# Kernel tuning notes

Measured on AMD Instinct MI355X. Metric: run time of the kernel, lower is better.

The kernel has to match this reference:

```python
import jax, jax.numpy as jnp
import numpy as np

D = 1024      # query_dim
H = 16        # heads
DH = 64       # dim_head
I = H * DH    # inner_dim = 1024
DC = 768      # context_dim
FF = 4 * D    # ff inner dim = 4096
EPS = 1e-5
SCALE = DH ** -0.5


def setup_inputs() -> dict:
    key = jax.random.key(0)
    ks = jax.random.split(key, 20)
    s = 0.02
    inp = {
        'x': jax.random.normal(ks[0], (2, 2048, D), jnp.float32),
        'context': jax.random.normal(ks[1], (2, 77, DC), jnp.float32),
        'ln1_g': jnp.ones((D,), jnp.float32), 'ln1_b': jnp.zeros((D,), jnp.float32),
        'ln2_g': jnp.ones((D,), jnp.float32), 'ln2_b': jnp.zeros((D,), jnp.float32),
        'ln3_g': jnp.ones((D,), jnp.float32), 'ln3_b': jnp.zeros((D,), jnp.float32),
        'Wq1': jax.random.normal(ks[2], (D, I), jnp.float32) * s,
        'Wk1': jax.random.normal(ks[3], (D, I), jnp.float32) * s,
        'Wv1': jax.random.normal(ks[4], (D, I), jnp.float32) * s,
        'Wo1': jax.random.normal(ks[5], (I, D), jnp.float32) * s,
        'bo1': jnp.zeros((D,), jnp.float32),
        'Wq2': jax.random.normal(ks[6], (D, I), jnp.float32) * s,
        'Wk2': jax.random.normal(ks[7], (DC, I), jnp.float32) * s,
        'Wv2': jax.random.normal(ks[8], (DC, I), jnp.float32) * s,
        'Wo2': jax.random.normal(ks[9], (I, D), jnp.float32) * s,
        'bo2': jnp.zeros((D,), jnp.float32),
        'Wff1': jax.random.normal(ks[10], (D, 2 * FF), jnp.float32) * s,
        'bff1': jnp.zeros((2 * FF,), jnp.float32),
        'Wff2': jax.random.normal(ks[11], (FF, D), jnp.float32) * s,
        'bff2': jnp.zeros((D,), jnp.float32),
    }
    return inp


def layer_norm(x, g, b):
    m = jnp.mean(x, axis=-1, keepdims=True)
    v = jnp.mean(jnp.square(x - m), axis=-1, keepdims=True)
    return (x - m) * jax.lax.rsqrt(v + EPS) * g + b


def cross_attention(x, ctx, Wq, Wk, Wv, Wo, bo):
    # x: [B,N,D], ctx: [B,M,Dc]
    B, N, _ = x.shape
    M = ctx.shape[1]
    q = (x @ Wq).reshape(B, N, H, DH).transpose(0, 2, 1, 3)    # [B,H,N,DH]
    k = (ctx @ Wk).reshape(B, M, H, DH).transpose(0, 2, 1, 3)  # [B,H,M,DH]
    v = (ctx @ Wv).reshape(B, M, H, DH).transpose(0, 2, 1, 3)
    sim = jnp.einsum('bhid,bhjd->bhij', q, k) * SCALE           # [B,H,N,M]
    attn = jax.nn.softmax(sim, axis=-1)
    out = jnp.einsum('bhij,bhjd->bhid', attn, v)                # [B,H,N,DH]
    out = out.transpose(0, 2, 1, 3).reshape(B, N, I)
    return out @ Wo + bo


def reference(x, context, ln1_g, ln1_b, ln2_g, ln2_b, ln3_g, ln3_b,
              Wq1, Wk1, Wv1, Wo1, bo1, Wq2, Wk2, Wv2, Wo2, bo2,
              Wff1, bff1, Wff2, bff2):
    # self-attention
    x = cross_attention(layer_norm(x, ln1_g, ln1_b), layer_norm(x, ln1_g, ln1_b),
                        Wq1, Wk1, Wv1, Wo1, bo1) + x
    # cross-attention
    x = cross_attention(layer_norm(x, ln2_g, ln2_b), context,
                        Wq2, Wk2, Wv2, Wo2, bo2) + x
    # GEGLU feed-forward
    hg = layer_norm(x, ln3_g, ln3_b) @ Wff1 + bff1
    h, gate = hg[..., :FF], hg[..., FF:]
    ff = (h * jax.nn.gelu(gate, approximate=False)) @ Wff2 + bff2
    return ff + x
```

## Files before the change

kernel.cpp:

```cpp
#include <hip/hip_runtime.h>
#include <hip/hip_bf16.h>
#include <math.h>

typedef short short8 __attribute__((ext_vector_type(8)));
typedef float floatx4 __attribute__((ext_vector_type(4)));
typedef unsigned short u16;

#define D_MODEL 1024
#define NH 16
#define DH 64
#define FF_DIM 4096

__device__ __forceinline__ u16 f2b(float f) {
  union { float f; unsigned u; } v; v.f = f;
  unsigned r = (v.u + 0x7fffu + ((v.u >> 16) & 1u)) >> 16;
  return (u16)r;
}
__device__ __forceinline__ u16 f2b_fast(float f) {
  union { float f; unsigned u; } v; v.f = f;
  return (u16)((v.u + 0x8000u) >> 16);
}
__device__ __forceinline__ float b2f(u16 h) {
  union { unsigned u; float f; } v; v.u = ((unsigned)h) << 16;
  return v.f;
}

__device__ __forceinline__ void gl_lds16(const u16* g, u16* l) {
  __builtin_amdgcn_global_load_lds(
      (const __attribute__((address_space(1))) unsigned int*)g,
      (__attribute__((address_space(3))) unsigned int*)l, 16, 0, 0);
}

__launch_bounds__(256)
__global__ void transpose_to_bf16(const float* __restrict__ in, u16* __restrict__ out,
                                  int K, int N, float scale) {
  __shared__ float tile[32][33];
  const int n0 = blockIdx.x * 32;
  const int k0 = blockIdx.y * 32;
  const int tx = threadIdx.x & 31;
  const int ty = threadIdx.x >> 5;
#pragma unroll
  for (int i = 0; i < 4; i++) {
    int k = k0 + ty + i * 8;
    tile[ty + i * 8][tx] = in[(size_t)k * N + (n0 + tx)] * scale;
  }
  __syncthreads();
#pragma unroll
  for (int i = 0; i < 4; i++) {
    int n = n0 + ty + i * 8;
    out[(size_t)n * K + (k0 + tx)] = f2b(tile[tx][ty + i * 8]);
  }
}

__launch_bounds__(256)
__global__ void convert_bf16(const float* __restrict__ in, u16* __restrict__ out, int n) {
  int i = blockIdx.x * 256 + threadIdx.x;
  if (i < n) out[i] = f2b(in[i]);
}

__launch_bounds__(256)
__global__ void ln_to_bf16(const float* __restrict__ x, const float* __restrict__ g,
                           const float* __restrict__ b, u16* __restrict__ out) {
  const int row = blockIdx.x;
  const int tid = threadIdx.x;
  const float4 v = ((const float4*)(x + (size_t)row * D_MODEL))[tid];
  float s = v.x + v.y + v.z + v.w;
  float ss = v.x * v.x + v.y * v.y + v.z * v.z + v.w * v.w;
#pragma unroll
  for (int o = 32; o; o >>= 1) { s += __shfl_xor(s, o); ss += __shfl_xor(ss, o); }
  __shared__ float red[8];
  const int wave = tid >> 6, lane = tid & 63;
  if (lane == 0) { red[wave] = s; red[4 + wave] = ss; }
  __syncthreads();
  const float st = red[0] + red[1] + red[2] + red[3];
  const float sst = red[4] + red[5] + red[6] + red[7];
  const float mean = st * (1.0f / D_MODEL);
  const float var = sst * (1.0f / D_MODEL) - mean * mean;
  const float rs = rsqrtf(var + 1e-5f);
  const float4 gv = ((const float4*)g)[tid];
  const float4 bv = ((const float4*)b)[tid];
  ushort4 o4;
  o4.x = f2b((v.x - mean) * rs * gv.x + bv.x);
  o4.y = f2b((v.y - mean) * rs * gv.y + bv.y);
  o4.z = f2b((v.z - mean) * rs * gv.z + bv.z);
  o4.w = f2b((v.w - mean) * rs * gv.w + bv.w);
  ((ushort4*)(out + (size_t)row * D_MODEL))[tid] = o4;
}

template <int EPI>
__launch_bounds__(256)
__global__ void gemm128(const u16* __restrict__ A, const u16* __restrict__ BT,
                        const float* __restrict__ bias, const float* __restrict__ resid,
                        float* __restrict__ Cf, u16* __restrict__ Cb, u16* __restrict__ VT,
                        int K, int lda, int ldb, int ldc) {
  __shared__ __attribute__((aligned(16))) u16 Al[128 * 32];
  __shared__ __attribute__((aligned(16))) u16 Bl[128 * 32];
  const int tid = threadIdx.x, wave = tid >> 6, lane = tid & 63;
  const int lm = lane & 15, lq = lane >> 4;
  const int wr = (wave >> 1) * 64, wc = (wave & 1) * 64;
  const int m0 = blockIdx.y * 128, n0 = blockIdx.x * 128;

  floatx4 acc[4][4] = {};

  for (int k0 = 0; k0 < K; k0 += 32) {
#pragma unroll
    for (int it = 0; it < 2; it++) {
      const int c = wave * 128 + it * 64 + lane;
      const int r = c >> 2, s = c & 3;
      gl_lds16(A + (size_t)(m0 + r) * lda + k0 + s * 8, &Al[c * 8]);
      gl_lds16(BT + (size_t)(n0 + r) * ldb + k0 + s * 8, &Bl[c * 8]);
    }
    __syncthreads();
    short8 af[4], bf[4];
#pragma unroll
    for (int r = 0; r < 4; r++) af[r] = *(const short8*)(&Al[(wr + r * 16 + lm) * 32 + lq * 8]);
#pragma unroll
    for (int c = 0; c < 4; c++) bf[c] = *(const short8*)(&Bl[(wc + c * 16 + lm) * 32 + lq * 8]);
#pragma unroll
    for (int r = 0; r < 4; r++)
#pragma unroll
      for (int c = 0; c < 4; c++)
        acc[r][c] = __builtin_amdgcn_mfma_f32_16x16x32_bf16(af[r], bf[c], acc[r][c], 0, 0, 0);
    __syncthreads();
  }

#pragma unroll
  for (int r = 0; r < 4; r++)
#pragma unroll
    for (int c = 0; c < 4; c++) {
      const int col = n0 + wc + c * 16 + lm;
      const int row0 = m0 + wr + r * 16 + lq * 4;
      if (EPI == 0) {
#pragma unroll
        for (int i = 0; i < 4; i++)
          Cb[(size_t)(row0 + i) * ldc + col] = f2b(acc[r][c][i]);
      } else if (EPI == 1) {
#pragma unroll
        for (int i = 0; i < 4; i++)
          Cf[(size_t)(row0 + i) * ldc + col] =
              acc[r][c][i] + bias[col] + resid[(size_t)(row0 + i) * ldc + col];
      } else {
        if (col < 2048) {
#pragma unroll
          for (int i = 0; i < 4; i++)
            Cb[(size_t)(row0 + i) * ldc + col] = f2b(acc[r][c][i]);
        } else {
          const int d = col - 2048;
          ushort4 pk;
          pk.x = f2b(acc[r][c][0]); pk.y = f2b(acc[r][c][1]);
          pk.z = f2b(acc[r][c][2]); pk.w = f2b(acc[r][c][3]);
          *(ushort4*)(&VT[((size_t)((row0 >> 11) * 1024 + d)) * 2048 + (row0 & 2047)]) = pk;
        }
      }
    }
}

__launch_bounds__(256)
__global__ void gemm_geglu(const u16* __restrict__ A, const u16* __restrict__ BT,
                           const float* __restrict__ bias, u16* __restrict__ Cb,
                           int K, int lda, int ldb) {
  __shared__ __attribute__((aligned(16))) u16 Al[128 * 32];
  __shared__ __attribute__((aligned(16))) u16 Bl[64 * 32];
  __shared__ __attribute__((aligned(16))) u16 Bg[64 * 32];
  const int tid = threadIdx.x, wave = tid >> 6, lane = tid & 63;
  const int lm = lane & 15, lq = lane >> 4;
  const int wr = (wave >> 1) * 64, wc = (wave & 1) * 32;
  const int m0 = blockIdx.y * 128, n0 = blockIdx.x * 64;

  floatx4 acc[4][2] = {};
  floatx4 accg[4][2] = {};

  for (int k0 = 0; k0 < K; k0 += 32) {
#pragma unroll
    for (int it = 0; it < 2; it++) {
      const int c = wave * 128 + it * 64 + lane;
      const int r = c >> 2, s = c & 3;
      gl_lds16(A + (size_t)(m0 + r) * lda + k0 + s * 8, &Al[c * 8]);
    }
    {
      const int c = wave * 64 + lane;
      const int r = c >> 2, s = c & 3;
      gl_lds16(BT + (size_t)(n0 + r) * ldb + k0 + s * 8, &Bl[c * 8]);
      gl_lds16(BT + (size_t)(n0 + r + FF_DIM) * ldb + k0 + s * 8, &Bg[c * 8]);
    }
    __syncthreads();
    short8 af[4], bf[2], bg[2];
#pragma unroll
    for (int r = 0; r < 4; r++) af[r] = *(const short8*)(&Al[(wr + r * 16 + lm) * 32 + lq * 8]);
#pragma unroll
    for (int c = 0; c < 2; c++) {
      bf[c] = *(const short8*)(&Bl[(wc + c * 16 + lm) * 32 + lq * 8]);
      bg[c] = *(const short8*)(&Bg[(wc + c * 16 + lm) * 32 + lq * 8]);
    }
#pragma unroll
    for (int r = 0; r < 4; r++)
#pragma unroll
      for (int c = 0; c < 2; c++) {
        acc[r][c] = __builtin_amdgcn_mfma_f32_16x16x32_bf16(af[r], bf[c], acc[r][c], 0, 0, 0);
        accg[r][c] = __builtin_amdgcn_mfma_f32_16x16x32_bf16(af[r], bg[c], accg[r][c], 0, 0, 0);
      }
    __syncthreads();
  }

#pragma unroll
  for (int r = 0; r < 4; r++)
#pragma unroll
    for (int c = 0; c < 2; c++) {
      const int col = n0 + wc + c * 16 + lm;
#pragma unroll
      for (int i = 0; i < 4; i++) {
        const int row = m0 + wr + r * 16 + lq * 4 + i;
        const float h = acc[r][c][i] + bias[col];
        const float gt = accg[r][c][i] + bias[col + FF_DIM];
        const float gl = 0.5f * gt * (1.0f + erff(gt * 0.70710678118f));
        Cb[(size_t)row * FF_DIM + col] = f2b(h * gl);
      }
    }
}

#define BM 64
#define BN 64
#define LSTR 40

template <int TRANS>
__launch_bounds__(256)
__global__ void gemm_bt64(const u16* __restrict__ A, const u16* __restrict__ BT,
                          u16* __restrict__ Cb,
                          int M, int N, int K, int lda, int ldb, int ldc, int rowsPerB) {
  __shared__ __attribute__((aligned(16))) u16 Al[BM * LSTR];
  __shared__ __attribute__((aligned(16))) u16 Bl[BN * LSTR];
  const int tid = threadIdx.x, wave = tid >> 6, lane = tid & 63;
  const int wm = (wave >> 1) * 32, wn = (wave & 1) * 32;
  const int lm = lane & 15, lq = lane >> 4;
  const int m0 = blockIdx.y * BM, n0 = blockIdx.x * BN;

  floatx4 acc[2][2] = {};
  const int srow = tid >> 2;
  const int scol = (tid & 3) * 8;
  const bool a_ok = (m0 + srow) < M;

  for (int k0 = 0; k0 < K; k0 += 32) {
    int4 av = make_int4(0, 0, 0, 0);
    if (a_ok) av = *(const int4*)(A + (size_t)(m0 + srow) * lda + k0 + scol);
    *(int4*)(&Al[srow * LSTR + scol]) = av;
    int4 bv = *(const int4*)(BT + (size_t)(n0 + srow) * ldb + k0 + scol);
    *(int4*)(&Bl[srow * LSTR + scol]) = bv;
    __syncthreads();
    short8 af[2], bfr[2];
#pragma unroll
    for (int r = 0; r < 2; r++) af[r] = *(const short8*)(&Al[(wm + r * 16 + lm) * LSTR + lq * 8]);
#pragma unroll
    for (int c = 0; c < 2; c++) bfr[c] = *(const short8*)(&Bl[(wn + c * 16 + lm) * LSTR + lq * 8]);
#pragma unroll
    for (int r = 0; r < 2; r++)
#pragma unroll
      for (int c = 0; c < 2; c++)
        acc[r][c] = __builtin_amdgcn_mfma_f32_16x16x32_bf16(af[r], bfr[c], acc[r][c], 0, 0, 0);
    __syncthreads();
  }

#pragma unroll
  for (int r = 0; r < 2; r++)
#pragma unroll
    for (int c = 0; c < 2; c++) {
      const int col = n0 + wn + c * 16 + lm;
#pragma unroll
      for (int i = 0; i < 4; i++) {
        const int row = m0 + wm + r * 16 + lq * 4 + i;
        if (row < M) {
          if (TRANS == 0) {
            Cb[(size_t)row * ldc + col] = f2b(acc[r][c][i]);
          } else {
            const int bb = row / rowsPerB;
            const int n = row - bb * rowsPerB;
            Cb[((size_t)(bb * 1024 + col)) * 128 + n] = f2b(acc[r][c][i]);
          }
        }
      }
    }
}

__launch_bounds__(256)
__global__ void attn_mfma(const u16* __restrict__ Qg, const u16* __restrict__ Kg,
                          const u16* __restrict__ VTg, u16* __restrict__ Ob,
                          int N, int Mk, int kRowsPerBatch, int ldq, int ldk, int vtld) {
  const int ntiles = N / 64;
  const int bh = blockIdx.x / ntiles;
  const int qt = blockIdx.x % ntiles;
  const int b = bh / NH, h = bh % NH;
  const int tid = threadIdx.x, wave = tid >> 6, lane = tid & 63;
  const int lm = lane & 15, lq = lane >> 4;

  __shared__ __attribute__((aligned(16))) u16 Qs[64 * 64];
  __shared__ __attribute__((aligned(16))) u16 Ks[64 * 64];
  __shared__ __attribute__((aligned(16))) u16 Vt[64 * 64];
  __shared__ __attribute__((aligned(16))) u16 Ps[4][16 * 72];

  const u16* Qh = Qg + (size_t)b * N * ldq + h * DH;
  const u16* Kh = Kg + (size_t)b * kRowsPerBatch * ldk + h * DH;
  const u16* Vh = VTg + (size_t)(b * 1024 + h * DH) * vtld;

  {
    const u16* qsrc = Qh + (size_t)qt * 64 * ldq;
#pragma unroll
    for (int it = 0; it < 2; it++) {
      const int c = wave * 128 + it * 64 + lane;
      const int r = c >> 3, p = c & 7, lc = p ^ (r & 7);
      gl_lds16(qsrc + (size_t)r * ldq + lc * 8, &Qs[c * 8]);
    }
  }
  __syncthreads();
  short8 qf[2];
  qf[0] = *(const short8*)(&Qs[(wave * 16 + lm) * 64 + ((lq) ^ (lm & 7)) * 8]);
  qf[1] = *(const short8*)(&Qs[(wave * 16 + lm) * 64 + ((4 + lq) ^ (lm & 7)) * 8]);

  float lpart[4] = {0.f, 0.f, 0.f, 0.f};
  floatx4 o[4] = {};

  for (int kt = 0; kt < Mk; kt += 64) {
    __syncthreads();
    {
      const u16* ksrc = Kh + (size_t)kt * ldk;
      const u16* vsrc = Vh + kt;
#pragma unroll
      for (int it = 0; it < 2; it++) {
        const int c = wave * 128 + it * 64 + lane;
        const int r = c >> 3, p = c & 7, lc = p ^ (r & 7);
        gl_lds16(ksrc + (size_t)r * ldk + lc * 8, &Ks[c * 8]);
        gl_lds16(vsrc + (size_t)r * vtld + lc * 8, &Vt[c * 8]);
      }
    }
    __syncthreads();

    floatx4 s[4];
#pragma unroll
    for (int ct = 0; ct < 4; ct++) {
      short8 kf0 = *(const short8*)(&Ks[(ct * 16 + lm) * 64 + ((lq) ^ (lm & 7)) * 8]);
      short8 kf1 = *(const short8*)(&Ks[(ct * 16 + lm) * 64 + ((4 + lq) ^ (lm & 7)) * 8]);
      floatx4 z = {};
      z = __builtin_amdgcn_mfma_f32_16x16x32_bf16(qf[0], kf0, z, 0, 0, 0);
      z = __builtin_amdgcn_mfma_f32_16x16x32_bf16(qf[1], kf1, z, 0, 0, 0);
      s[ct] = z;
    }

    if (kt + 64 <= Mk) {
#pragma unroll
      for (int reg = 0; reg < 4; reg++) {
        float p0 = __expf(s[0][reg] - 16.0f);
        float p1 = __expf(s[1][reg] - 16.0f);
        float p2 = __expf(s[2][reg] - 16.0f);
        float p3 = __expf(s[3][reg] - 16.0f);
        lpart[reg] += (p0 + p1) + (p2 + p3);
        const int prow = (lq * 4 + reg) * 72;
        Ps[wave][prow + lm] = f2b_fast(p0);
        Ps[wave][prow + 16 + lm] = f2b_fast(p1);
        Ps[wave][prow + 32 + lm] = f2b_fast(p2);
        Ps[wave][prow + 48 + lm] = f2b_fast(p3);
      }
    } else {
#pragma unroll
      for (int reg = 0; reg < 4; reg++) {
        const int prow = (lq * 4 + reg) * 72;
        float psum = 0.f;
#pragma unroll
        for (int ct = 0; ct < 4; ct++) {
          const bool valid = (kt + ct * 16 + lm) < Mk;
          float p = valid ? __expf(s[ct][reg] - 16.0f) : 0.f;
          psum += p;
          Ps[wave][prow + ct * 16 + lm] = f2b_fast(p);
        }
        lpart[reg] += psum;
      }
    }

    const short8 pf0 = *(const short8*)(&Ps[wave][lm * 72 + lq * 8]);
    const short8 pf1 = *(const short8*)(&Ps[wave][lm * 72 + 32 + lq * 8]);
#pragma unroll
    for (int ct = 0; ct < 4; ct++) {
      short8 vf0 = *(const short8*)(&Vt[(ct * 16 + lm) * 64 + ((lq) ^ (lm & 7)) * 8]);
      short8 vf1 = *(const short8*)(&Vt[(ct * 16 + lm) * 64 + ((4 + lq) ^ (lm & 7)) * 8]);
      o[ct] = __builtin_amdgcn_mfma_f32_16x16x32_bf16(pf0, vf0, o[ct], 0, 0, 0);
      o[ct] = __builtin_amdgcn_mfma_f32_16x16x32_bf16(pf1, vf1, o[ct], 0, 0, 0);
    }
  }

  float inv[4];
#pragma unroll
  for (int reg = 0; reg < 4; reg++) {
    float l = lpart[reg];
    l += __shfl_xor(l, 1); l += __shfl_xor(l, 2);
    l += __shfl_xor(l, 4); l += __shfl_xor(l, 8);
    inv[reg] = 1.0f / l;
  }
#pragma unroll
  for (int ct = 0; ct < 4; ct++)
#pragma unroll
    for (int reg = 0; reg < 4; reg++) {
      const int grow = qt * 64 + wave * 16 + lq * 4 + reg;
      Ob[((size_t)(b * N + grow)) * D_MODEL + h * DH + ct * 16 + lm] =
          f2b(o[ct][reg] * inv[reg]);
    }
}

extern "C" void kernel_launch(void* const* d_in, const int* in_sizes, int n_in,
                              void* d_out, int out_size, void* d_ws, size_t ws_size,
                              hipStream_t stream) {
  const float* x    = (const float*)d_in[0];
  const float* ctx  = (const float*)d_in[1];
  const float* ln1g = (const float*)d_in[2];
  const float* ln1b = (const float*)d_in[3];
  const float* ln2g = (const float*)d_in[4];
  const float* ln2b = (const float*)d_in[5];
  const float* ln3g = (const float*)d_in[6];
  const float* ln3b = (const float*)d_in[7];
  const float* Wq1  = (const float*)d_in[8];
  const float* Wk1  = (const float*)d_in[9];
  const float* Wv1  = (const float*)d_in[10];
  const float* Wo1  = (const float*)d_in[11];
  const float* bo1  = (const float*)d_in[12];
  const float* Wq2  = (const float*)d_in[13];
  const float* Wk2  = (const float*)d_in[14];
  const float* Wv2  = (const float*)d_in[15];
  const float* Wo2  = (const float*)d_in[16];
  const float* bo2  = (const float*)d_in[17];
  const float* Wff1 = (const float*)d_in[18];
  const float* bff1 = (const float*)d_in[19];
  const float* Wff2 = (const float*)d_in[20];
  const float* bff2 = (const float*)d_in[21];
  float* out = (float*)d_out;

  char* ws = (char*)d_ws;
  size_t off = 0;
  auto alloc = [&](size_t bytes) -> char* {
    char* p = ws + off;
    off += (bytes + 255) & ~(size_t)255;
    return p;
  };
  u16* wqkv1T = (u16*)alloc((size_t)3072 * 1024 * 2);
  u16* wo1T   = (u16*)alloc((size_t)1024 * 1024 * 2);
  u16* wq2T   = (u16*)alloc((size_t)1024 * 1024 * 2);
  u16* wk2T   = (u16*)alloc((size_t)1024 * 768 * 2);
  u16* wv2T   = (u16*)alloc((size_t)1024 * 768 * 2);
  u16* wo2T   = (u16*)alloc((size_t)1024 * 1024 * 2);
  u16* wff1T  = (u16*)alloc((size_t)8192 * 1024 * 2);
  u16* wff2T  = (u16*)alloc((size_t)1024 * 4096 * 2);
  u16* xln    = (u16*)alloc((size_t)4096 * 1024 * 2);
  u16* ctxb   = (u16*)alloc((size_t)154 * 768 * 2);
  u16* QKVb   = (u16*)alloc((size_t)4096 * 3072 * 2);
  u16* VTb    = (u16*)alloc((size_t)2048 * 2048 * 2);
  u16* K2b    = (u16*)alloc((size_t)256 * 1024 * 2);
  u16* VT2b   = (u16*)alloc((size_t)2048 * 128 * 2);
  u16* Ob     = (u16*)alloc((size_t)4096 * 1024 * 2);
  float* x1   = (float*)alloc((size_t)4096 * 1024 * 4);
  float* x2   = (float*)alloc((size_t)4096 * 1024 * 4);
  u16* ffin   = (u16*)alloc((size_t)4096 * 4096 * 2);
  u16* Q2b    = ffin;

  dim3 blk(256);

  transpose_to_bf16<<<dim3(32, 32), blk, 0, stream>>>(Wq1, wqkv1T, 1024, 1024, 1.0f);
  transpose_to_bf16<<<dim3(32, 32), blk, 0, stream>>>(Wk1, wqkv1T + (size_t)1024 * 1024, 1024, 1024, 0.125f);
  transpose_to_bf16<<<dim3(32, 32), blk, 0, stream>>>(Wv1, wqkv1T + (size_t)2048 * 1024, 1024, 1024, 1.0f);
  transpose_to_bf16<<<dim3(32, 32), blk, 0, stream>>>(Wo1, wo1T, 1024, 1024, 1.0f);
  transpose_to_bf16<<<dim3(32, 32), blk, 0, stream>>>(Wq2, wq2T, 1024, 1024, 1.0f);
  transpose_to_bf16<<<dim3(32, 24), blk, 0, stream>>>(Wk2, wk2T, 768, 1024, 0.125f);
  transpose_to_bf16<<<dim3(32, 24), blk, 0, stream>>>(Wv2, wv2T, 768, 1024, 1.0f);
  transpose_to_bf16<<<dim3(32, 32), blk, 0, stream>>>(Wo2, wo2T, 1024, 1024, 1.0f);
  transpose_to_bf16<<<dim3(256, 32), blk, 0, stream>>>(Wff1, wff1T, 1024, 8192, 1.0f);
  transpose_to_bf16<<<dim3(32, 128), blk, 0, stream>>>(Wff2, wff2T, 4096, 1024, 1.0f);
  convert_bf16<<<(154 * 768 + 255) / 256, blk, 0, stream>>>(ctx, ctxb, 154 * 768);

  ln_to_bf16<<<4096, blk, 0, stream>>>(x, ln1g, ln1b, xln);
  gemm128<2><<<dim3(24, 32), blk, 0, stream>>>(xln, wqkv1T, nullptr, nullptr, nullptr, QKVb,
                                               VTb, 1024, 1024, 1024, 3072);
  attn_mfma<<<2 * NH * (2048 / 64), blk, 0, stream>>>(QKVb, QKVb + 1024, VTb, Ob,
                                                      2048, 2048, 2048, 3072, 3072, 2048);
  gemm128<1><<<dim3(8, 32), blk, 0, stream>>>(Ob, wo1T, bo1, x, x1, nullptr, nullptr,
                                              1024, 1024, 1024, 1024);

  ln_to_bf16<<<4096, blk, 0, stream>>>(x1, ln2g, ln2b, xln);
  gemm128<0><<<dim3(8, 32), blk, 0, stream>>>(xln, wq2T, nullptr, nullptr, nullptr, Q2b,
                                              nullptr, 1024, 1024, 1024, 1024);
  gemm_bt64<0><<<dim3(16, 3), blk, 0, stream>>>(ctxb, wk2T, K2b, 154, 1024, 768, 768, 768, 1024, 77);
  gemm_bt64<1><<<dim3(16, 3), blk, 0, stream>>>(ctxb, wv2T, VT2b, 154, 1024, 768, 768, 768, 1024, 77);
  attn_mfma<<<2 * NH * (2048 / 64), blk, 0, stream>>>(Q2b, K2b, VT2b, Ob,
                                                      2048, 77, 77, 1024, 1024, 128);
  gemm128<1><<<dim3(8, 32), blk, 0, stream>>>(Ob, wo2T, bo2, x1, x2, nullptr, nullptr,
                                              1024, 1024, 1024, 1024);

  ln_to_bf16<<<4096, blk, 0, stream>>>(x2, ln3g, ln3b, xln);
  gemm_geglu<<<dim3(64, 32), blk, 0, stream>>>(xln, wff1T, bff1, ffin, 1024, 1024, 1024);
  gemm128<1><<<dim3(8, 32), blk, 0, stream>>>(ffin, wff2T, bff2, x2, out, nullptr, nullptr,
                                              4096, 4096, 4096, 1024);
}
```

Before: 606.8 us.

## Pre-swizzle weights into MFMA fragment layout and load B directly to registers

All weight transposes and the context conversion are merged into one prep kernel. It writes weights in a per-lane MFMA fragment-tiled layout, so the GEMMs load B operands straight from global memory into registers with one step of double buffering, with no LDS staging for B. The GEGLU epilogue swaps exact erf GELU for the tanh approximation written as a sigmoid via __expf, which changes numerics slightly. It also reallocates buffers so Q2 gets its own buffer and ffin reuses QKVb.

After: 639.1 us. 1.05x slower.

```diff
diff --git a/kernel.cpp b/kernel.cpp
--- a/kernel.cpp
+++ b/kernel.cpp
@@ -11,6 +11,14 @@
 #define DH 64
 #define FF_DIM 4096
 
+#define O_QKV 0
+#define O_O1  3145728
+#define O_Q2  4194304
+#define O_O2  5242880
+#define O_FF1 6291456
+#define O_FF2 14680064
+#define WS_TOTAL 18874368
+
 __device__ __forceinline__ u16 f2b(float f) {
   union { float f; unsigned u; } v; v.f = f;
   unsigned r = (v.u + 0x7fffu + ((v.u >> 16) & 1u)) >> 16;
@@ -20,10 +28,6 @@
   union { float f; unsigned u; } v; v.f = f;
   return (u16)((v.u + 0x8000u) >> 16);
 }
-__device__ __forceinline__ float b2f(u16 h) {
-  union { unsigned u; float f; } v; v.u = ((unsigned)h) << 16;
-  return v.f;
-}
 
 __device__ __forceinline__ void gl_lds16(const u16* g, u16* l) {
   __builtin_amdgcn_global_load_lds(
@@ -32,30 +36,71 @@
 }
 
 __launch_bounds__(256)
-__global__ void transpose_to_bf16(const float* __restrict__ in, u16* __restrict__ out,
-                                  int K, int N, float scale) {
-  __shared__ float tile[32][33];
-  const int n0 = blockIdx.x * 32;
-  const int k0 = blockIdx.y * 32;
-  const int tx = threadIdx.x & 31;
-  const int ty = threadIdx.x >> 5;
-#pragma unroll
-  for (int i = 0; i < 4; i++) {
-    int k = k0 + ty + i * 8;
-    tile[ty + i * 8][tx] = in[(size_t)k * N + (n0 + tx)] * scale;
-  }
-  __syncthreads();
-#pragma unroll
-  for (int i = 0; i < 4; i++) {
-    int n = n0 + ty + i * 8;
-    out[(size_t)n * K + (k0 + tx)] = f2b(tile[tx][ty + i * 8]);
-  }
-}
-
-__launch_bounds__(256)
-__global__ void convert_bf16(const float* __restrict__ in, u16* __restrict__ out, int n) {
-  int i = blockIdx.x * 256 + threadIdx.x;
-  if (i < n) out[i] = f2b(in[i]);
+__global__ void prep_all(const float* __restrict__ Wq1, const float* __restrict__ Wk1,
+                         const float* __restrict__ Wv1, const float* __restrict__ Wo1,
+                         const float* __restrict__ Wq2, const float* __restrict__ Wo2,
+                         const float* __restrict__ Wff1, const float* __restrict__ Wff2,
+                         const float* __restrict__ Wk2, const float* __restrict__ Wv2,
+                         const float* __restrict__ ctx,
+                         u16* __restrict__ ws, u16* __restrict__ wk2T,
+                         u16* __restrict__ wv2T, u16* __restrict__ ctxb) {
+  const int p = blockIdx.x * 4 + (threadIdx.x >> 6);
+  const int lane = threadIdx.x & 63;
+  const int lm = lane & 15, lq = lane >> 4;
+  union { short8 v; u16 u[8]; } ob;
+
+  if (p < 6144) {
+    const int pl = p, kt = pl & 31;
+    const int n = (pl >> 5) * 16 + lm, k0 = kt * 32 + lq * 8;
+    const float* src; int nl; float s;
+    if (n < 1024) { src = Wq1; nl = n; s = 1.f; }
+    else if (n < 2048) { src = Wk1; nl = n - 1024; s = 0.125f; }
+    else { src = Wv1; nl = n - 2048; s = 1.f; }
+#pragma unroll
+    for (int j = 0; j < 8; j++) ob.u[j] = f2b(src[(size_t)(k0 + j) * 1024 + nl] * s);
+    *(short8*)(ws + O_QKV + (size_t)pl * 512 + lane * 8) = ob.v;
+  } else if (p < 12288) {
+    const int pl = (p - 6144) & 2047;
+    const int which = (p - 6144) >> 11;
+    const float* src = (which == 0) ? Wo1 : (which == 1) ? Wq2 : Wo2;
+    const size_t dof = (which == 0) ? O_O1 : (which == 1) ? O_Q2 : O_O2;
+    const int kt = pl & 31;
+    const int n = (pl >> 5) * 16 + lm, k0 = kt * 32 + lq * 8;
+#pragma unroll
+    for (int j = 0; j < 8; j++) ob.u[j] = f2b(src[(size_t)(k0 + j) * 1024 + n]);
+    *(short8*)(ws + dof + (size_t)pl * 512 + lane * 8) = ob.v;
+  } else if (p < 28672) {
+    const int pl = p - 12288;
+    const int kt = pl & 31;
+    const int n = (pl >> 5) * 16 + lm, k0 = kt * 32 + lq * 8;
+#pragma unroll
+    for (int j = 0; j < 8; j++) ob.u[j] = f2b(Wff1[(size_t)(k0 + j) * 8192 + n]);
+    *(short8*)(ws + O_FF1 + (size_t)pl * 512 + lane * 8) = ob.v;
+  } else if (p < 36864) {
+    const int pl = p - 28672;
+    const int kt = pl & 127;
+    const int n = (pl >> 7) * 16 + lm, k0 = kt * 32 + lq * 8;
+#pragma unroll
+    for (int j = 0; j < 8; j++) ob.u[j] = f2b(Wff2[(size_t)(k0 + j) * 1024 + n]);
+    *(short8*)(ws + O_FF2 + (size_t)pl * 512 + lane * 8) = ob.v;
+  } else if (p < 39936) {
+    const int pl = (p - 36864) % 1536;
+    const bool isK = (p - 36864) < 1536;
+    const float* src = isK ? Wk2 : Wv2;
+    const float s = isK ? 0.125f : 1.f;
+    u16* dst = isK ? wk2T : wv2T;
+    const int nt = pl / 24, kt = pl - nt * 24;
+    const int n = nt * 16 + lm, k0 = kt * 32 + lq * 8;
+#pragma unroll
+    for (int j = 0; j < 8; j++) ob.u[j] = f2b(src[(size_t)(k0 + j) * 1024 + n] * s);
+    *(short8*)(dst + (size_t)n * 768 + k0) = ob.v;
+  } else if (p < 40167) {
+    const int pl = p - 39936;
+    const size_t idx = (size_t)pl * 512 + lane * 8;
+#pragma unroll
+    for (int j = 0; j < 8; j++) ob.u[j] = f2b(ctx[idx + j]);
+    *(short8*)(ctxb + idx) = ob.v;
+  }
 }
 
 __launch_bounds__(256)
@@ -89,38 +134,65 @@
 
 template <int EPI>
 __launch_bounds__(256)
-__global__ void gemm128(const u16* __restrict__ A, const u16* __restrict__ BT,
+__global__ void gemm128(const u16* __restrict__ A, const u16* __restrict__ WS,
                         const float* __restrict__ bias, const float* __restrict__ resid,
                         float* __restrict__ Cf, u16* __restrict__ Cb, u16* __restrict__ VT,
-                        int K, int lda, int ldb, int ldc) {
+                        int KT, int lda, int ldc) {
   __shared__ __attribute__((aligned(16))) u16 Al[128 * 32];
-  __shared__ __attribute__((aligned(16))) u16 Bl[128 * 32];
   const int tid = threadIdx.x, wave = tid >> 6, lane = tid & 63;
   const int lm = lane & 15, lq = lane >> 4;
   const int wr = (wave >> 1) * 64, wc = (wave & 1) * 64;
   const int m0 = blockIdx.y * 128, n0 = blockIdx.x * 128;
 
+  const u16* wsb = WS + ((size_t)((n0 >> 4) + (wave & 1) * 4) * KT) * 512 + lane * 8;
   floatx4 acc[4][4] = {};
-
-  for (int k0 = 0; k0 < K; k0 += 32) {
+  short8 b0[4], b1[4];
+
+#pragma unroll
+  for (int c = 0; c < 4; c++) b0[c] = *(const short8*)(wsb + (size_t)(c * KT) * 512);
+
+  for (int kt = 0; kt < KT; kt += 2) {
 #pragma unroll
     for (int it = 0; it < 2; it++) {
       const int c = wave * 128 + it * 64 + lane;
       const int r = c >> 2, s = c & 3;
-      gl_lds16(A + (size_t)(m0 + r) * lda + k0 + s * 8, &Al[c * 8]);
-      gl_lds16(BT + (size_t)(n0 + r) * ldb + k0 + s * 8, &Bl[c * 8]);
-    }
-    __syncthreads();
-    short8 af[4], bf[4];
-#pragma unroll
-    for (int r = 0; r < 4; r++) af[r] = *(const short8*)(&Al[(wr + r * 16 + lm) * 32 + lq * 8]);
-#pragma unroll
-    for (int c = 0; c < 4; c++) bf[c] = *(const short8*)(&Bl[(wc + c * 16 + lm) * 32 + lq * 8]);
-#pragma unroll
-    for (int r = 0; r < 4; r++)
-#pragma unroll
-      for (int c = 0; c < 4; c++)
-        acc[r][c] = __builtin_amdgcn_mfma_f32_16x16x32_bf16(af[r], bf[c], acc[r][c], 0, 0, 0);
+      gl_lds16(A + (size_t)(m0 + r) * lda + kt * 32 + s * 8, &Al[c * 8]);
+    }
+#pragma unroll
+    for (int c = 0; c < 4; c++) b1[c] = *(const short8*)(wsb + (size_t)(c * KT + kt + 1) * 512);
+    __syncthreads();
+    {
+      short8 af[4];
+#pragma unroll
+      for (int r = 0; r < 4; r++) af[r] = *(const short8*)(&Al[(wr + r * 16 + lm) * 32 + lq * 8]);
+#pragma unroll
+      for (int r = 0; r < 4; r++)
+#pragma unroll
+        for (int c = 0; c < 4; c++)
+          acc[r][c] = __builtin_amdgcn_mfma_f32_16x16x32_bf16(af[r], b0[c], acc[r][c], 0, 0, 0);
+    }
+    __syncthreads();
+#pragma unroll
+    for (int it = 0; it < 2; it++) {
+      const int c = wave * 128 + it * 64 + lane;
+      const int r = c >> 2, s = c & 3;
+      gl_lds16(A + (size_t)(m0 + r) * lda + (kt + 1) * 32 + s * 8, &Al[c * 8]);
+    }
+    if (kt + 2 < KT) {
+#pragma unroll
+      for (int c = 0; c < 4; c++) b0[c] = *(const short8*)(wsb + (size_t)(c * KT + kt + 2) * 512);
+    }
+    __syncthreads();
+    {
+      short8 af[4];
+#pragma unroll
+      for (int r = 0; r < 4; r++) af[r] = *(const short8*)(&Al[(wr + r * 16 + lm) * 32 + lq * 8]);
+#pragma unroll
+      for (int r = 0; r < 4; r++)
+#pragma unroll
+        for (int c = 0; c < 4; c++)
+          acc[r][c] = __builtin_amdgcn_mfma_f32_16x16x32_bf16(af[r], b1[c], acc[r][c], 0, 0, 0);
+    }
     __syncthreads();
   }
 
@@ -156,49 +228,79 @@
 }
 
 __launch_bounds__(256)
-__global__ void gemm_geglu(const u16* __restrict__ A, const u16* __restrict__ BT,
+__global__ void gemm_geglu(const u16* __restrict__ A, const u16* __restrict__ WS,
                            const float* __restrict__ bias, u16* __restrict__ Cb,
-                           int K, int lda, int ldb) {
+                           int KT, int lda) {
   __shared__ __attribute__((aligned(16))) u16 Al[128 * 32];
-  __shared__ __attribute__((aligned(16))) u16 Bl[64 * 32];
-  __shared__ __attribute__((aligned(16))) u16 Bg[64 * 32];
   const int tid = threadIdx.x, wave = tid >> 6, lane = tid & 63;
   const int lm = lane & 15, lq = lane >> 4;
   const int wr = (wave >> 1) * 64, wc = (wave & 1) * 32;
   const int m0 = blockIdx.y * 128, n0 = blockIdx.x * 64;
 
+  const u16* wsh = WS + ((size_t)((n0 >> 4) + (wave & 1) * 2) * KT) * 512 + lane * 8;
+  const u16* wsg = wsh + (size_t)256 * KT * 512;
   floatx4 acc[4][2] = {};
   floatx4 accg[4][2] = {};
-
-  for (int k0 = 0; k0 < K; k0 += 32) {
+  short8 bh0[2], bg0[2], bh1[2], bg1[2];
+
+#pragma unroll
+  for (int c = 0; c < 2; c++) {
+    bh0[c] = *(const short8*)(wsh + (size_t)(c * KT) * 512);
+    bg0[c] = *(const short8*)(wsg + (size_t)(c * KT) * 512);
+  }
+
+  for (int kt = 0; kt < KT; kt += 2) {
 #pragma unroll
     for (int it = 0; it < 2; it++) {
       const int c = wave * 128 + it * 64 + lane;
       const int r = c >> 2, s = c & 3;
-      gl_lds16(A + (size_t)(m0 + r) * lda + k0 + s * 8, &Al[c * 8]);
-    }
+      gl_lds16(A + (size_t)(m0 + r) * lda + kt * 32 + s * 8, &Al[c * 8]);
+    }
+#pragma unroll
+    for (int c = 0; c < 2; c++) {
+      bh1[c] = *(const short8*)(wsh + (size_t)(c * KT + kt + 1) * 512);
+      bg1[c] = *(const short8*)(wsg + (size_t)(c * KT + kt + 1) * 512);
+    }
+    __syncthreads();
     {
-      const int c = wave * 64 + lane;
+      short8 af[4];
+#pragma unroll
+      for (int r = 0; r < 4; r++) af[r] = *(const short8*)(&Al[(wr + r * 16 + lm) * 32 + lq * 8]);
+#pragma unroll
+      for (int r = 0; r < 4; r++)
+#pragma unroll
+        for (int c = 0; c < 2; c++) {
+          acc[r][c] = __builtin_amdgcn_mfma_f32_16x16x32_bf16(af[r], bh0[c], acc[r][c], 0, 0, 0);
+          accg[r][c] = __builtin_amdgcn_mfma_f32_16x16x32_bf16(af[r], bg0[c], accg[r][c], 0, 0, 0);
+        }
+    }
+    __syncthreads();
+#pragma unroll
+    for (int it = 0; it < 2; it++) {
+      const int c = wave * 128 + it * 64 + lane;
       const int r = c >> 2, s = c & 3;
-      gl_lds16(BT + (size_t)(n0 + r) * ldb + k0 + s * 8, &Bl[c * 8]);
-      gl_lds16(BT + (size_t)(n0 + r + FF_DIM) * ldb + k0 + s * 8, &Bg[c * 8]);
-    }
-    __syncthreads();
-    short8 af[4], bf[2], bg[2];
-#pragma unroll
-    for (int r = 0; r < 4; r++) af[r] = *(const short8*)(&Al[(wr + r * 16 + lm) * 32 + lq * 8]);
-#pragma unroll
-    for (int c = 0; c < 2; c++) {
-      bf[c] = *(const short8*)(&Bl[(wc + c * 16 + lm) * 32 + lq * 8]);
-      bg[c] = *(const short8*)(&Bg[(wc + c * 16 + lm) * 32 + lq * 8]);
-    }
-#pragma unroll
-    for (int r = 0; r < 4; r++)
+      gl_lds16(A + (size_t)(m0 + r) * lda + (kt + 1) * 32 + s * 8, &Al[c * 8]);
+    }
+    if (kt + 2 < KT) {
 #pragma unroll
       for (int c = 0; c < 2; c++) {
-        acc[r][c] = __builtin_amdgcn_mfma_f32_16x16x32_bf16(af[r], bf[c], acc[r][c], 0, 0, 0);
-        accg[r][c] = __builtin_amdgcn_mfma_f32_16x16x32_bf16(af[r], bg[c], accg[r][c], 0, 0, 0);
-      }
+        bh0[c] = *(const short8*)(wsh + (size_t)(c * KT + kt + 2) * 512);
+        bg0[c] = *(const short8*)(wsg + (size_t)(c * KT + kt + 2) * 512);
+      }
+    }
+    __syncthreads();
+    {
+      short8 af[4];
+#pragma unroll
+      for (int r = 0; r < 4; r++) af[r] = *(const short8*)(&Al[(wr + r * 16 + lm) * 32 + lq * 8]);
+#pragma unroll
+      for (int r = 0; r < 4; r++)
+#pragma unroll
+        for (int c = 0; c < 2; c++) {
+          acc[r][c] = __builtin_amdgcn_mfma_f32_16x16x32_bf16(af[r], bh1[c], acc[r][c], 0, 0, 0);
+          accg[r][c] = __builtin_amdgcn_mfma_f32_16x16x32_bf16(af[r], bg1[c], accg[r][c], 0, 0, 0);
+        }
+    }
     __syncthreads();
   }
 
@@ -212,7 +314,8 @@
         const int row = m0 + wr + r * 16 + lq * 4 + i;
         const float h = acc[r][c][i] + bias[col];
         const float gt = accg[r][c][i] + bias[col + FF_DIM];
-        const float gl = 0.5f * gt * (1.0f + erff(gt * 0.70710678118f));
+        const float z = 1.5957691216f * (gt + 0.044715f * gt * gt * gt);
+        const float gl = gt / (1.0f + __expf(-z));
         Cb[(size_t)row * FF_DIM + col] = f2b(h * gl);
       }
     }
@@ -305,7 +408,7 @@
 #pragma unroll
     for (int it = 0; it < 2; it++) {
       const int c = wave * 128 + it * 64 + lane;
-      const int r = c >> 3, p = c & 7, lc = p ^ (r & 7);
+      const int r = c >> 3, pp = c & 7, lc = pp ^ (r & 7);
       gl_lds16(qsrc + (size_t)r * ldq + lc * 8, &Qs[c * 8]);
     }
   }
@@ -325,7 +428,7 @@
 #pragma unroll
       for (int it = 0; it < 2; it++) {
         const int c = wave * 128 + it * 64 + lane;
-        const int r = c >> 3, p = c & 7, lc = p ^ (r & 7);
+        const int r = c >> 3, pp = c & 7, lc = pp ^ (r & 7);
         gl_lds16(ksrc + (size_t)r * ldk + lc * 8, &Ks[c * 8]);
         gl_lds16(vsrc + (size_t)r * vtld + lc * 8, &Vt[c * 8]);
       }
@@ -365,9 +468,9 @@
 #pragma unroll
         for (int ct = 0; ct < 4; ct++) {
           const bool valid = (kt + ct * 16 + lm) < Mk;
-          float p = valid ? __expf(s[ct][reg] - 16.0f) : 0.f;
-          psum += p;
-          Ps[wave][prow + ct * 16 + lm] = f2b_fast(p);
+          float pv = valid ? __expf(s[ct][reg] - 16.0f) : 0.f;
+          psum += pv;
+          Ps[wave][prow + ct * 16 + lm] = f2b_fast(pv);
         }
         lpart[reg] += psum;
       }
@@ -436,60 +539,46 @@
     off += (bytes + 255) & ~(size_t)255;
     return p;
   };
-  u16* wqkv1T = (u16*)alloc((size_t)3072 * 1024 * 2);
-  u16* wo1T   = (u16*)alloc((size_t)1024 * 1024 * 2);
-  u16* wq2T   = (u16*)alloc((size_t)1024 * 1024 * 2);
-  u16* wk2T   = (u16*)alloc((size_t)1024 * 768 * 2);
-  u16* wv2T   = (u16*)alloc((size_t)1024 * 768 * 2);
-  u16* wo2T   = (u16*)alloc((size_t)1024 * 1024 * 2);
-  u16* wff1T  = (u16*)alloc((size_t)8192 * 1024 * 2);
-  u16* wff2T  = (u16*)alloc((size_t)1024 * 4096 * 2);
-  u16* xln    = (u16*)alloc((size_t)4096 * 1024 * 2);
-  u16* ctxb   = (u16*)alloc((size_t)154 * 768 * 2);
-  u16* QKVb   = (u16*)alloc((size_t)4096 * 3072 * 2);
-  u16* VTb    = (u16*)alloc((size_t)2048 * 2048 * 2);
-  u16* K2b    = (u16*)alloc((size_t)256 * 1024 * 2);
-  u16* VT2b   = (u16*)alloc((size_t)2048 * 128 * 2);
-  u16* Ob     = (u16*)alloc((size_t)4096 * 1024 * 2);
-  float* x1   = (float*)alloc((size_t)4096 * 1024 * 4);
-  float* x2   = (float*)alloc((size_t)4096 * 1024 * 4);
-  u16* ffin   = (u16*)alloc((size_t)4096 * 4096 * 2);
-  u16* Q2b    = ffin;
+  u16* wsAll = (u16*)alloc((size_t)WS_TOTAL * 2);
+  u16* wk2T  = (u16*)alloc((size_t)1024 * 768 * 2);
+  u16* wv2T  = (u16*)alloc((size_t)1024 * 768 * 2);
+  u16* ctxb  = (u16*)alloc((size_t)154 * 768 * 2);
+  u16* xln   = (u16*)alloc((size_t)4096 * 1024 * 2);
+  u16* QKVb  = (u16*)alloc((size_t)4096 * 3072 * 2);
+  u16* VTb   = (u16*)alloc((size_t)2048 * 2048 * 2);
+  u16* K2b   = (u16*)alloc((size_t)256 * 1024 * 2);
+  u16* VT2b  = (u16*)alloc((size_t)2048 * 128 * 2);
+  u16* Ob    = (u16*)alloc((size_t)4096 * 1024 * 2);
+  u16* Q2b   = (u16*)alloc((size_t)4096 * 1024 * 2);
+  float* x1  = (float*)alloc((size_t)4096 * 1024 * 4);
+  float* x2  = (float*)alloc((size_t)4096 * 1024 * 4);
+  u16* ffin  = QKVb;
 
   dim3 blk(256);
 
-  transpose_to_bf16<<<dim3(32, 32), blk, 0, stream>>>(Wq1, wqkv1T, 1024, 1024, 1.0f);
-  transpose_to_bf16<<<dim3(32, 32), blk, 0, stream>>>(Wk1, wqkv1T + (size_t)1024 * 1024, 1024, 1024, 0.125f);
-  transpose_to_bf16<<<dim3(32, 32), blk, 0, stream>>>(Wv1, wqkv1T + (size_t)2048 * 1024, 1024, 1024, 1.0f);
-  transpose_to_bf16<<<dim3(32, 32), blk, 0, stream>>>(Wo1, wo1T, 1024, 1024, 1.0f);
-  transpose_to_bf16<<<dim3(32, 32), blk, 0, stream>>>(Wq2, wq2T, 1024, 1024, 1.0f);
-  transpose_to_bf16<<<dim3(32, 24), blk, 0, stream>>>(Wk2, wk2T, 768, 1024, 0.125f);
-  transpose_to_bf16<<<dim3(32, 24), blk, 0, stream>>>(Wv2, wv2T, 768, 1024, 1.0f);
-  transpose_to_bf16<<<dim3(32, 32), blk, 0, stream>>>(Wo2, wo2T, 1024, 1024, 1.0f);
-  transpose_to_bf16<<<dim3(256, 32), blk, 0, stream>>>(Wff1, wff1T, 1024, 8192, 1.0f);
-  transpose_to_bf16<<<dim3(32, 128), blk, 0, stream>>>(Wff2, wff2T, 4096, 1024, 1.0f);
-  convert_bf16<<<(154 * 768 + 255) / 256, blk, 0, stream>>>(ctx, ctxb, 154 * 768);
+  prep_all<<<10042, blk, 0, stream>>>(Wq1, Wk1, Wv1, Wo1, Wq2, Wo2, Wff1, Wff2,
+                                      Wk2, Wv2, ctx, wsAll, wk2T, wv2T, ctxb);
 
   ln_to_bf16<<<4096, blk, 0, stream>>>(x, ln1g, ln1b, xln);
-  gemm128<2><<<dim3(24, 32), blk, 0, stream>>>(xln, wqkv1T, nullptr, nullptr, nullptr, QKVb,
-                                               VTb, 1024, 1024, 1024, 3072);
+  gemm128<2><<<dim3(24, 32), blk, 0, stream>>>(xln, wsAll + O_QKV, nullptr, nullptr,
+                                               nullptr, QKVb, VTb, 32, 1024, 3072);
   attn_mfma<<<2 * NH * (2048 / 64), blk, 0, stream>>>(QKVb, QKVb + 1024, VTb, Ob,
                                                       2048, 2048, 2048, 3072, 3072, 2048);
-  gemm128<1><<<dim3(8, 32), blk, 0, stream>>>(Ob, wo1T, bo1, x, x1, nullptr, nullptr,
-                                              1024, 1024, 1024, 1024);
+  gemm128<1><<<dim3(8, 32), blk, 0, stream>>>(Ob, wsAll + O_O1, bo1, x, x1, nullptr,
+                                              nullptr, 32, 1024, 1024);
 
   ln_to_bf16<<<4096, blk, 0, stream>>>(x1, ln2g, ln2b, xln);
-  gemm128<0><<<dim3(8, 32), blk, 0, stream>>>(xln, wq2T, nullptr, nullptr, nullptr, Q2b,
-                                              nullptr, 1024, 1024, 1024, 1024);
+  gemm128<0><<<dim3(8, 32), blk, 0, stream>>>(xln, wsAll + O_Q2, nullptr, nullptr,
+                                              nullptr, Q2b, nullptr, 32, 1024, 1024);
   gemm_bt64<0><<<dim3(16, 3), blk, 0, stream>>>(ctxb, wk2T, K2b, 154, 1024, 768, 768, 768, 1024, 77);
   gemm_bt64<1><<<dim3(16, 3), blk, 0, stream>>>(ctxb, wv2T, VT2b, 154, 1024, 768, 768, 768, 1024, 77);
   attn_mfma<<<2 * NH * (2048 / 64), blk, 0, stream>>>(Q2b, K2b, VT2b, Ob,
                                                       2048, 77, 77, 1024, 1024, 128);
-  gemm128<1><<<dim3(8, 32), blk, 0, stream>>>(Ob, wo2T, bo2, x1, x2, nullptr, nullptr,
-                                              1024, 1024, 1024, 1024);
+  gemm128<1><<<dim3(8, 32), blk, 0, stream>>>(Ob, wsAll + O_O2, bo2, x1, x2, nullptr,
+                                              nullptr, 32, 1024, 1024);
 
   ln_to_bf16<<<4096, blk, 0, stream>>>(x2, ln3g, ln3b, xln);
-  gemm_geglu<<<dim3(64, 32), blk, 0, stream>>>(xln, wff1T, bff1, ffin, 1024, 1024, 1024);
-  gemm128<1><<<dim3(8, 32), blk, 0, stream>>>(ffin, wff2T, bff2, x2, out, nullptr, nullptr,
-                                              4096, 4096, 4096, 1024);
-}
+  gemm_geglu<<<dim3(64, 32), blk, 0, stream>>>(xln, wsAll + O_FF1, bff1, ffin, 32, 1024);
+  gemm128<1><<<dim3(8, 32), blk, 0, stream>>>(ffin, wsAll + O_FF2, bff2, x2, out,
+                                              nullptr, nullptr, 128, 4096, 1024);
+}
```
